# Optimization experiments

Hardware: AMD Instinct MI355X
Metric: run time of the kernel (lower is better)

## Reference

```python
import jax, jax.numpy as jnp
import numpy as np

D = 1024      # model dim
F = 4 * D     # FFN hidden dim
E = 8         # number of experts
TOP_K = 2


def setup_inputs() -> dict:
    key = jax.random.key(0)
    ks = jax.random.split(key, 7)
    s_r = 1.0 / np.sqrt(D)
    s_f = 1.0 / np.sqrt(F)
    return {
        "x": jax.random.normal(ks[0], (2, 2048, D), dtype=jnp.float32),
        "Wr": jax.random.uniform(ks[1], (D, E), jnp.float32, -s_r, s_r),
        "br": jax.random.uniform(ks[2], (E,), jnp.float32, -s_r, s_r),
        "W1": jax.random.uniform(ks[3], (E, D, F), jnp.float32, -s_r, s_r),
        "b1": jax.random.uniform(ks[4], (E, F), jnp.float32, -s_r, s_r),
        "W2": jax.random.uniform(ks[5], (E, F, D), jnp.float32, -s_f, s_f),
        "b2": jax.random.uniform(ks[6], (E, D), jnp.float32, -s_f, s_f),
    }


def reference(x, Wr, br, W1, b1, W2, b2):
    B, S, d = x.shape
    T = B * S
    xf = x.reshape(T, d)                                   # [T, D]
    logits = xf @ Wr + br                                  # [T, E]
    top_vals, top_idx = jax.lax.top_k(logits, TOP_K)       # [T, K]
    rw = jax.nn.softmax(top_vals, axis=-1)                 # softmax over selected experts
    # Dense routing-weight matrix: zero for unselected experts -> same math as masked loop.
    w = jnp.zeros((T, E), dtype=xf.dtype).at[jnp.arange(T)[:, None], top_idx].add(rw)  # [T, E]
    # All-expert FFN (exact GELU to match torch.nn.GELU default).
    h = jax.nn.gelu(jnp.einsum('td,edf->tef', xf, W1) + b1[None], approximate=False)   # [T, E, F]
    y = jnp.einsum('tef,efd->ted', h, W2) + b2[None]       # [T, E, D]
    out = jnp.einsum('te,ted->td', w, y)                   # combine
    return out.reshape(B, S, d)
```

## Files before the change

### kernel.cpp

```cpp
#include <hip/hip_runtime.h>
#include <math.h>


#define T_TOK 4096
#define DMODEL 1024
#define FDIM 4096
#define NEXP 8
#define MAXROWS 9216
#define NRB 72

typedef unsigned short u16;
typedef unsigned int u32;
typedef __attribute__((ext_vector_type(8))) short short8;
typedef __attribute__((ext_vector_type(4))) float f32x4;

constexpr size_t OFF_CTRL   = 0;
constexpr size_t OFF_ROWMAP = 4096;
constexpr size_t OFF_ROWW   = OFF_ROWMAP + (size_t)MAXROWS*4;
constexpr size_t OFF_TKIDX  = OFF_ROWW + (size_t)MAXROWS*4;
constexpr size_t OFF_TKW    = OFF_TKIDX + (size_t)T_TOK*2*4;
constexpr size_t OFF_XB     = 262144;
constexpr size_t OFF_W1T    = OFF_XB + (size_t)T_TOK*DMODEL*2;
constexpr size_t OFF_W2T    = OFF_W1T + (size_t)NEXP*DMODEL*FDIM*2;
constexpr size_t OFF_H      = OFF_W2T + (size_t)NEXP*FDIM*DMODEL*2;
constexpr size_t WS_NEED    = OFF_H + (size_t)MAXROWS*FDIM*2;

__device__ __forceinline__ u16 f2bf(float f) {
  u32 u = __float_as_uint(f);
  u += 0x7FFFu + ((u >> 16) & 1u);
  return (u16)(u >> 16);
}

__device__ __forceinline__ float fast_gelu(float v) {
  float u2 = v * (1.5957691216f + 0.0713548162f * v * v);
  float s = __expf(-u2);
  return v * __builtin_amdgcn_rcpf(1.0f + s);
}

__device__ __forceinline__ void async16(void* lds, const void* g) {
  __builtin_amdgcn_global_load_lds((const __attribute__((address_space(1))) void*)g,
                                   (__attribute__((address_space(3))) void*)lds,
                                   16, 0, 0);
}

__global__ void init_cast_kernel(const float* __restrict__ x, u16* __restrict__ xb,
                                 int* __restrict__ ctrl, int* __restrict__ rowmap) {
  int g = blockIdx.x * 256 + threadIdx.x;
  float4 v = ((const float4*)x)[g];
  u32 p0 = (u32)f2bf(v.x) | ((u32)f2bf(v.y) << 16);
  u32 p1 = (u32)f2bf(v.z) | ((u32)f2bf(v.w) << 16);
  ((uint2*)xb)[g] = make_uint2(p0, p1);
  if (g < NEXP) ctrl[g] = 0;
  if (g < MAXROWS) rowmap[g] = -1;
}

__global__ void router_kernel(const float* __restrict__ x, const float* __restrict__ Wr,
                              const float* __restrict__ br, int* __restrict__ ctrl,
                              int* __restrict__ tk_idx, float* __restrict__ tk_w) {
  int lane = threadIdx.x & 63, w = threadIdx.x >> 6;
  int t = blockIdx.x * 4 + w;
  const float* xt = x + (size_t)t * DMODEL;
  float acc[8] = {0.f,0.f,0.f,0.f,0.f,0.f,0.f,0.f};
  for (int i = 0; i < DMODEL / 64; i++) {
    int d = i * 64 + lane;
    float xv = xt[d];
    float4 w0 = *(const float4*)(Wr + d * 8);
    float4 w1 = *(const float4*)(Wr + d * 8 + 4);
    acc[0] += xv * w0.x; acc[1] += xv * w0.y; acc[2] += xv * w0.z; acc[3] += xv * w0.w;
    acc[4] += xv * w1.x; acc[5] += xv * w1.y; acc[6] += xv * w1.z; acc[7] += xv * w1.w;
  }
  #pragma unroll
  for (int off = 32; off > 0; off >>= 1)
    #pragma unroll
    for (int e = 0; e < 8; e++) acc[e] += __shfl_xor(acc[e], off);
  if (lane == 0) {
    float lg[8];
    #pragma unroll
    for (int e = 0; e < 8; e++) lg[e] = acc[e] + br[e];
    int e0 = 0;
    #pragma unroll
    for (int e = 1; e < 8; e++) if (lg[e] > lg[e0]) e0 = e;
    int e1 = -1;
    #pragma unroll
    for (int e = 0; e < 8; e++) if (e != e0 && (e1 < 0 || lg[e] > lg[e1])) e1 = e;
    float p1 = __expf(lg[e1] - lg[e0]);
    float inv = 1.f / (1.f + p1);
    tk_idx[t*2] = e0; tk_idx[t*2+1] = e1;
    tk_w[t*2] = inv;  tk_w[t*2+1] = p1 * inv;
    atomicAdd(&ctrl[e0], 1); atomicAdd(&ctrl[e1], 1);
  }
}

__global__ void transpose_cast_kernel(const float* __restrict__ in, u16* __restrict__ outp,
                                      int K, int N) {
  __shared__ float tile[64][65];
  int e = blockIdx.z;
  const float* src = in + (size_t)e * K * N;
  u16* dst = outp + (size_t)e * K * N;
  int k0 = blockIdx.y * 64, n0 = blockIdx.x * 64;
  int t = threadIdx.x;
  int kr = t >> 4, nc = (t & 15) * 4;
  #pragma unroll
  for (int rr = 0; rr < 4; rr++) {
    int k = kr + rr * 16;
    float4 v = *(const float4*)(src + (size_t)(k0 + k) * N + n0 + nc);
    tile[nc+0][k] = v.x; tile[nc+1][k] = v.y; tile[nc+2][k] = v.z; tile[nc+3][k] = v.w;
  }
  __syncthreads();
  int n = t >> 2, kc = (t & 3) * 16;
  u32 res[8];
  #pragma unroll
  for (int u = 0; u < 8; u++) {
    u32 lo = f2bf(tile[n][kc + u*2]);
    u32 hi = f2bf(tile[n][kc + u*2 + 1]);
    res[u] = lo | (hi << 16);
  }
  uint4* o = (uint4*)(dst + (size_t)(n0 + n) * K + k0 + kc);
  o[0] = make_uint4(res[0], res[1], res[2], res[3]);
  o[1] = make_uint4(res[4], res[5], res[6], res[7]);
}

__global__ void scan_kernel(int* __restrict__ ctrl) {
  __shared__ int so[9];
  if (threadIdx.x == 0) {
    int o = 0;
    for (int e = 0; e < 8; e++) {
      so[e] = o; ctrl[16 + e] = o;
      o += (ctrl[e] + 127) & ~127;
    }
    so[8] = o; ctrl[24] = o;
    for (int e = 0; e < 8; e++) ctrl[8 + e] = 0;
  }
  __syncthreads();
  int b = threadIdx.x;
  if (b < NRB) {
    int base = b * 128, ex = -1;
    for (int e = 0; e < 8; e++) if (base >= so[e] && base < so[e+1]) ex = e;
    ctrl[32 + b] = ex;
  }
}

__global__ void assign_kernel(const int* __restrict__ tk_idx, const float* __restrict__ tk_w,
                              int* __restrict__ ctrl, int* __restrict__ rowmap,
                              float* __restrict__ roww) {
  int t = blockIdx.x * 256 + threadIdx.x;
  if (t >= T_TOK) return;
  #pragma unroll
  for (int k = 0; k < 2; k++) {
    int e = tk_idx[t*2 + k];
    int slot = atomicAdd(&ctrl[8 + e], 1);
    int r = ctrl[16 + e] + slot;
    rowmap[r] = t;
    roww[r] = tk_w[t*2 + k];
  }
}


__global__ void gemm1_kernel(const u16* __restrict__ xb, const u16* __restrict__ W1t,
                             const float* __restrict__ b1, const int* __restrict__ ctrl,
                             const int* __restrict__ rowmap, u16* __restrict__ h) {
  int rb = blockIdx.y, nb = blockIdx.x;
  int e = ctrl[32 + rb];
  if (e < 0) return;
  __shared__ u16 As[4096];
  __shared__ u16 Bs[4096];
  int tid = threadIdx.x, lane = tid & 63, w = tid >> 6;
  int c0 = w, c1 = w + 4;
  int rA0 = c0*16 + (lane >> 2), rA1 = c1*16 + (lane >> 2);
  int colo = (((lane & 3) ^ ((lane >> 3) & 3))) * 8;
  int t0 = rowmap[rb*128 + rA0]; t0 = t0 < 0 ? 0 : t0;
  int t1 = rowmap[rb*128 + rA1]; t1 = t1 < 0 ? 0 : t1;
  const u16* gA0 = xb + (size_t)t0 * DMODEL + colo;
  const u16* gA1 = xb + (size_t)t1 * DMODEL + colo;
  const u16* We  = W1t + (size_t)e * FDIM * DMODEL;
  const u16* gB0 = We + (size_t)(nb*128 + rA0) * DMODEL + colo;
  const u16* gB1 = We + (size_t)(nb*128 + rA1) * DMODEL + colo;
  u16* lA0 = &As[c0*512]; u16* lA1 = &As[c1*512];
  u16* lB0 = &Bs[c0*512]; u16* lB1 = &Bs[c1*512];
  f32x4 acc[4][4];
  f32x4 z = {0.f, 0.f, 0.f, 0.f};
  #pragma unroll
  for (int i = 0; i < 4; i++)
    #pragma unroll
    for (int j = 0; j < 4; j++) acc[i][j] = z;
  int m0 = (w >> 1) * 64, n0 = (w & 1) * 64, q = lane >> 4, cc = lane & 15;
  int sa = (q ^ ((cc >> 1) & 3)) * 8;
  for (int kb = 0; kb < DMODEL / 32; kb++) {
    async16(lA0, gA0); async16(lA1, gA1);
    async16(lB0, gB0); async16(lB1, gB1);
    gA0 += 32; gA1 += 32; gB0 += 32; gB1 += 32;
    __syncthreads();
    short8 af[4], bf[4];
    #pragma unroll
    for (int i = 0; i < 4; i++) af[i] = *(const short8*)&As[(m0 + i*16 + cc)*32 + sa];
    #pragma unroll
    for (int j = 0; j < 4; j++) bf[j] = *(const short8*)&Bs[(n0 + j*16 + cc)*32 + sa];
    #pragma unroll
    for (int i = 0; i < 4; i++)
      #pragma unroll
      for (int j = 0; j < 4; j++)
        acc[i][j] = __builtin_amdgcn_mfma_f32_16x16x32_bf16(af[i], bf[j], acc[i][j], 0, 0, 0);
    __syncthreads();
  }
  float bias[4];
  #pragma unroll
  for (int j = 0; j < 4; j++) bias[j] = b1[e*FDIM + nb*128 + n0 + j*16 + cc];
  #pragma unroll
  for (int i = 0; i < 4; i++)
    #pragma unroll
    for (int j = 0; j < 4; j++) {
      int col = nb*128 + n0 + j*16 + cc;
      #pragma unroll
      for (int r = 0; r < 4; r++) {
        int row = rb*128 + m0 + i*16 + q*4 + r;
        float v = acc[i][j][r] + bias[j];
        h[(size_t)row * FDIM + col] = f2bf(fast_gelu(v));
      }
    }
}

__global__ void gemm2_kernel(const u16* __restrict__ h, const u16* __restrict__ W2t,
                             const float* __restrict__ b2, const int* __restrict__ ctrl,
                             const int* __restrict__ rowmap, const float* __restrict__ roww,
                             float* __restrict__ out) {
  int rb = blockIdx.y, nb = blockIdx.x, zs = blockIdx.z;
  int e = ctrl[32 + rb];
  if (e < 0) return;
  __shared__ u16 As[4096];
  __shared__ u16 Bs[4096];
  int tid = threadIdx.x, lane = tid & 63, w = tid >> 6;
  int c0 = w, c1 = w + 4;
  int rA0 = c0*16 + (lane >> 2), rA1 = c1*16 + (lane >> 2);
  int colo = (((lane & 3) ^ ((lane >> 3) & 3))) * 8;
  size_t kbase = (size_t)zs * (FDIM / 2);
  const u16* gA0 = h + (size_t)(rb*128 + rA0) * FDIM + kbase + colo;
  const u16* gA1 = h + (size_t)(rb*128 + rA1) * FDIM + kbase + colo;
  const u16* We  = W2t + (size_t)e * DMODEL * FDIM;
  const u16* gB0 = We + (size_t)(nb*128 + rA0) * FDIM + kbase + colo;
  const u16* gB1 = We + (size_t)(nb*128 + rA1) * FDIM + kbase + colo;
  u16* lA0 = &As[c0*512]; u16* lA1 = &As[c1*512];
  u16* lB0 = &Bs[c0*512]; u16* lB1 = &Bs[c1*512];
  f32x4 acc[4][4];
  f32x4 z = {0.f, 0.f, 0.f, 0.f};
  #pragma unroll
  for (int i = 0; i < 4; i++)
    #pragma unroll
    for (int j = 0; j < 4; j++) acc[i][j] = z;
  int m0 = (w >> 1) * 64, n0 = (w & 1) * 64, q = lane >> 4, cc = lane & 15;
  int sa = (q ^ ((cc >> 1) & 3)) * 8;
  for (int kb = 0; kb < FDIM / 2 / 32; kb++) {
    async16(lA0, gA0); async16(lA1, gA1);
    async16(lB0, gB0); async16(lB1, gB1);
    gA0 += 32; gA1 += 32; gB0 += 32; gB1 += 32;
    __syncthreads();
    short8 af[4], bf[4];
    #pragma unroll
    for (int i = 0; i < 4; i++) af[i] = *(const short8*)&As[(m0 + i*16 + cc)*32 + sa];
    #pragma unroll
    for (int j = 0; j < 4; j++) bf[j] = *(const short8*)&Bs[(n0 + j*16 + cc)*32 + sa];
    #pragma unroll
    for (int i = 0; i < 4; i++)
      #pragma unroll
      for (int j = 0; j < 4; j++)
        acc[i][j] = __builtin_amdgcn_mfma_f32_16x16x32_bf16(af[i], bf[j], acc[i][j], 0, 0, 0);
    __syncthreads();
  }
  float bias[4];
  #pragma unroll
  for (int j = 0; j < 4; j++)
    bias[j] = (zs == 0) ? b2[e*DMODEL + nb*128 + n0 + j*16 + cc] : 0.0f;
  #pragma unroll
  for (int i = 0; i < 4; i++)
    #pragma unroll
    for (int r = 0; r < 4; r++) {
      int row = rb*128 + m0 + i*16 + q*4 + r;
      int t = rowmap[row];
      if (t < 0) continue;
      float wgt = roww[row];
      float* orow = out + (size_t)t * DMODEL;
      #pragma unroll
      for (int j = 0; j < 4; j++) {
        int col = nb*128 + n0 + j*16 + cc;
        atomicAdd(orow + col, wgt * (acc[i][j][r] + bias[j]));
      }
    }
}

extern "C" void kernel_launch(void* const* d_in, const int* in_sizes, int n_in,
                              void* d_out, int out_size, void* d_ws, size_t ws_size,
                              hipStream_t stream) {
  const float* x  = (const float*)d_in[0];
  const float* Wr = (const float*)d_in[1];
  const float* br = (const float*)d_in[2];
  const float* W1 = (const float*)d_in[3];
  const float* b1 = (const float*)d_in[4];
  const float* W2 = (const float*)d_in[5];
  const float* b2 = (const float*)d_in[6];
  float* out = (float*)d_out;
  char* ws = (char*)d_ws;
  if (ws_size < WS_NEED) return;

  int*   ctrl   = (int*)(ws + OFF_CTRL);
  int*   rowmap = (int*)(ws + OFF_ROWMAP);
  float* roww   = (float*)(ws + OFF_ROWW);
  int*   tk_idx = (int*)(ws + OFF_TKIDX);
  float* tk_w   = (float*)(ws + OFF_TKW);
  u16*   xb     = (u16*)(ws + OFF_XB);
  u16*   W1t    = (u16*)(ws + OFF_W1T);
  u16*   W2t    = (u16*)(ws + OFF_W2T);
  u16*   hbuf   = (u16*)(ws + OFF_H);

  hipMemsetAsync(out, 0, (size_t)out_size * sizeof(float), stream);
  init_cast_kernel<<<T_TOK*DMODEL/4/256, 256, 0, stream>>>(x, xb, ctrl, rowmap);
  router_kernel<<<T_TOK/4, 256, 0, stream>>>(x, Wr, br, ctrl, tk_idx, tk_w);
  transpose_cast_kernel<<<dim3(FDIM/64, DMODEL/64, NEXP), 256, 0, stream>>>(W1, W1t, DMODEL, FDIM);
  transpose_cast_kernel<<<dim3(DMODEL/64, FDIM/64, NEXP), 256, 0, stream>>>(W2, W2t, FDIM, DMODEL);
  scan_kernel<<<1, 128, 0, stream>>>(ctrl);
  assign_kernel<<<T_TOK/256, 256, 0, stream>>>(tk_idx, tk_w, ctrl, rowmap, roww);
  gemm1_kernel<<<dim3(FDIM/128, NRB), 256, 0, stream>>>(xb, W1t, b1, ctrl, rowmap, hbuf);
  gemm2_kernel<<<dim3(DMODEL/128, NRB, 2), 256, 0, stream>>>(hbuf, W2t, b2, ctrl, rowmap, roww, out);
}
```

Before: 744.3 us.

## Double-buffer GEMM LDS tiles and replace atomic split-K scatter with a combine pass

Both expert GEMMs now use two LDS buffers per operand. Each k-step issues the async global-to-LDS loads for the next tile before running the MFMAs on the current one, and only one barrier remains per iteration. gemm2 drops its two-way split-K and float atomicAdd scatter into the output: it runs the full K loop and writes per-row expert outputs to a y buffer placed over the W1t workspace. A new combine kernel then gathers each token's two rows through a token-to-row map and applies the routing weights, which also removes the output memset. The cost is that gemm2 launches half as many blocks, and there is an extra fp32 write and read of the y buffer.

```diff
diff --git a/kernel.cpp b/kernel.cpp
--- a/kernel.cpp
+++ b/kernel.cpp
@@ -19,11 +19,13 @@
 constexpr size_t OFF_ROWW   = OFF_ROWMAP + (size_t)MAXROWS*4;
 constexpr size_t OFF_TKIDX  = OFF_ROWW + (size_t)MAXROWS*4;
 constexpr size_t OFF_TKW    = OFF_TKIDX + (size_t)T_TOK*2*4;
+constexpr size_t OFF_T2R    = OFF_TKW + (size_t)T_TOK*2*4;
 constexpr size_t OFF_XB     = 262144;
 constexpr size_t OFF_W1T    = OFF_XB + (size_t)T_TOK*DMODEL*2;
 constexpr size_t OFF_W2T    = OFF_W1T + (size_t)NEXP*DMODEL*FDIM*2;
 constexpr size_t OFF_H      = OFF_W2T + (size_t)NEXP*FDIM*DMODEL*2;
 constexpr size_t WS_NEED    = OFF_H + (size_t)MAXROWS*FDIM*2;
+constexpr size_t OFF_Y      = OFF_W1T;
 
 __device__ __forceinline__ u16 f2bf(float f) {
   u32 u = __float_as_uint(f);
@@ -142,7 +144,7 @@
 
 __global__ void assign_kernel(const int* __restrict__ tk_idx, const float* __restrict__ tk_w,
                               int* __restrict__ ctrl, int* __restrict__ rowmap,
-                              float* __restrict__ roww) {
+                              float* __restrict__ roww, int* __restrict__ t2r) {
   int t = blockIdx.x * 256 + threadIdx.x;
   if (t >= T_TOK) return;
   #pragma unroll
@@ -152,6 +154,7 @@
     int r = ctrl[16 + e] + slot;
     rowmap[r] = t;
     roww[r] = tk_w[t*2 + k];
+    t2r[t*2 + k] = r;
   }
 }
 
@@ -162,8 +165,8 @@
   int rb = blockIdx.y, nb = blockIdx.x;
   int e = ctrl[32 + rb];
   if (e < 0) return;
-  __shared__ u16 As[4096];
-  __shared__ u16 Bs[4096];
+  __shared__ u16 As[2][4096];
+  __shared__ u16 Bs[2][4096];
   int tid = threadIdx.x, lane = tid & 63, w = tid >> 6;
   int c0 = w, c1 = w + 4;
   int rA0 = c0*16 + (lane >> 2), rA1 = c1*16 + (lane >> 2);
@@ -175,8 +178,6 @@
   const u16* We  = W1t + (size_t)e * FDIM * DMODEL;
   const u16* gB0 = We + (size_t)(nb*128 + rA0) * DMODEL + colo;
   const u16* gB1 = We + (size_t)(nb*128 + rA1) * DMODEL + colo;
-  u16* lA0 = &As[c0*512]; u16* lA1 = &As[c1*512];
-  u16* lB0 = &Bs[c0*512]; u16* lB1 = &Bs[c1*512];
   f32x4 acc[4][4];
   f32x4 z = {0.f, 0.f, 0.f, 0.f};
   #pragma unroll
@@ -185,22 +186,29 @@
     for (int j = 0; j < 4; j++) acc[i][j] = z;
   int m0 = (w >> 1) * 64, n0 = (w & 1) * 64, q = lane >> 4, cc = lane & 15;
   int sa = (q ^ ((cc >> 1) & 3)) * 8;
-  for (int kb = 0; kb < DMODEL / 32; kb++) {
-    async16(lA0, gA0); async16(lA1, gA1);
-    async16(lB0, gB0); async16(lB1, gB1);
-    gA0 += 32; gA1 += 32; gB0 += 32; gB1 += 32;
+  async16(&As[0][c0*512], gA0); async16(&As[0][c1*512], gA1);
+  async16(&Bs[0][c0*512], gB0); async16(&Bs[0][c1*512], gB1);
+  gA0 += 32; gA1 += 32; gB0 += 32; gB1 += 32;
+  constexpr int NK = DMODEL / 32;
+  for (int kb = 0; kb < NK; kb++) {
+    int cur = kb & 1;
     __syncthreads();
+    if (kb + 1 < NK) {
+      int nxt = cur ^ 1;
+      async16(&As[nxt][c0*512], gA0); async16(&As[nxt][c1*512], gA1);
+      async16(&Bs[nxt][c0*512], gB0); async16(&Bs[nxt][c1*512], gB1);
+      gA0 += 32; gA1 += 32; gB0 += 32; gB1 += 32;
+    }
     short8 af[4], bf[4];
     #pragma unroll
-    for (int i = 0; i < 4; i++) af[i] = *(const short8*)&As[(m0 + i*16 + cc)*32 + sa];
-    #pragma unroll
-    for (int j = 0; j < 4; j++) bf[j] = *(const short8*)&Bs[(n0 + j*16 + cc)*32 + sa];
+    for (int i = 0; i < 4; i++) af[i] = *(const short8*)&As[cur][(m0 + i*16 + cc)*32 + sa];
+    #pragma unroll
+    for (int j = 0; j < 4; j++) bf[j] = *(const short8*)&Bs[cur][(n0 + j*16 + cc)*32 + sa];
     #pragma unroll
     for (int i = 0; i < 4; i++)
       #pragma unroll
       for (int j = 0; j < 4; j++)
         acc[i][j] = __builtin_amdgcn_mfma_f32_16x16x32_bf16(af[i], bf[j], acc[i][j], 0, 0, 0);
-    __syncthreads();
   }
   float bias[4];
   #pragma unroll
@@ -221,25 +229,21 @@
 
 __global__ void gemm2_kernel(const u16* __restrict__ h, const u16* __restrict__ W2t,
                              const float* __restrict__ b2, const int* __restrict__ ctrl,
-                             const int* __restrict__ rowmap, const float* __restrict__ roww,
-                             float* __restrict__ out) {
-  int rb = blockIdx.y, nb = blockIdx.x, zs = blockIdx.z;
+                             float* __restrict__ y) {
+  int rb = blockIdx.y, nb = blockIdx.x;
   int e = ctrl[32 + rb];
   if (e < 0) return;
-  __shared__ u16 As[4096];
-  __shared__ u16 Bs[4096];
+  __shared__ u16 As[2][4096];
+  __shared__ u16 Bs[2][4096];
   int tid = threadIdx.x, lane = tid & 63, w = tid >> 6;
   int c0 = w, c1 = w + 4;
   int rA0 = c0*16 + (lane >> 2), rA1 = c1*16 + (lane >> 2);
   int colo = (((lane & 3) ^ ((lane >> 3) & 3))) * 8;
-  size_t kbase = (size_t)zs * (FDIM / 2);
-  const u16* gA0 = h + (size_t)(rb*128 + rA0) * FDIM + kbase + colo;
-  const u16* gA1 = h + (size_t)(rb*128 + rA1) * FDIM + kbase + colo;
+  const u16* gA0 = h + (size_t)(rb*128 + rA0) * FDIM + colo;
+  const u16* gA1 = h + (size_t)(rb*128 + rA1) * FDIM + colo;
   const u16* We  = W2t + (size_t)e * DMODEL * FDIM;
-  const u16* gB0 = We + (size_t)(nb*128 + rA0) * FDIM + kbase + colo;
-  const u16* gB1 = We + (size_t)(nb*128 + rA1) * FDIM + kbase + colo;
-  u16* lA0 = &As[c0*512]; u16* lA1 = &As[c1*512];
-  u16* lB0 = &Bs[c0*512]; u16* lB1 = &Bs[c1*512];
+  const u16* gB0 = We + (size_t)(nb*128 + rA0) * FDIM + colo;
+  const u16* gB1 = We + (size_t)(nb*128 + rA1) * FDIM + colo;
   f32x4 acc[4][4];
   f32x4 z = {0.f, 0.f, 0.f, 0.f};
   #pragma unroll
@@ -248,42 +252,58 @@
     for (int j = 0; j < 4; j++) acc[i][j] = z;
   int m0 = (w >> 1) * 64, n0 = (w & 1) * 64, q = lane >> 4, cc = lane & 15;
   int sa = (q ^ ((cc >> 1) & 3)) * 8;
-  for (int kb = 0; kb < FDIM / 2 / 32; kb++) {
-    async16(lA0, gA0); async16(lA1, gA1);
-    async16(lB0, gB0); async16(lB1, gB1);
-    gA0 += 32; gA1 += 32; gB0 += 32; gB1 += 32;
+  async16(&As[0][c0*512], gA0); async16(&As[0][c1*512], gA1);
+  async16(&Bs[0][c0*512], gB0); async16(&Bs[0][c1*512], gB1);
+  gA0 += 32; gA1 += 32; gB0 += 32; gB1 += 32;
+  constexpr int NK = FDIM / 32;
+  for (int kb = 0; kb < NK; kb++) {
+    int cur = kb & 1;
     __syncthreads();
+    if (kb + 1 < NK) {
+      int nxt = cur ^ 1;
+      async16(&As[nxt][c0*512], gA0); async16(&As[nxt][c1*512], gA1);
+      async16(&Bs[nxt][c0*512], gB0); async16(&Bs[nxt][c1*512], gB1);
+      gA0 += 32; gA1 += 32; gB0 += 32; gB1 += 32;
+    }
     short8 af[4], bf[4];
     #pragma unroll
-    for (int i = 0; i < 4; i++) af[i] = *(const short8*)&As[(m0 + i*16 + cc)*32 + sa];
-    #pragma unroll
-    for (int j = 0; j < 4; j++) bf[j] = *(const short8*)&Bs[(n0 + j*16 + cc)*32 + sa];
+    for (int i = 0; i < 4; i++) af[i] = *(const short8*)&As[cur][(m0 + i*16 + cc)*32 + sa];
+    #pragma unroll
+    for (int j = 0; j < 4; j++) bf[j] = *(const short8*)&Bs[cur][(n0 + j*16 + cc)*32 + sa];
     #pragma unroll
     for (int i = 0; i < 4; i++)
       #pragma unroll
       for (int j = 0; j < 4; j++)
         acc[i][j] = __builtin_amdgcn_mfma_f32_16x16x32_bf16(af[i], bf[j], acc[i][j], 0, 0, 0);
-    __syncthreads();
   }
   float bias[4];
   #pragma unroll
-  for (int j = 0; j < 4; j++)
-    bias[j] = (zs == 0) ? b2[e*DMODEL + nb*128 + n0 + j*16 + cc] : 0.0f;
+  for (int j = 0; j < 4; j++) bias[j] = b2[e*DMODEL + nb*128 + n0 + j*16 + cc];
   #pragma unroll
   for (int i = 0; i < 4; i++)
     #pragma unroll
     for (int r = 0; r < 4; r++) {
       int row = rb*128 + m0 + i*16 + q*4 + r;
-      int t = rowmap[row];
-      if (t < 0) continue;
-      float wgt = roww[row];
-      float* orow = out + (size_t)t * DMODEL;
+      float* yrow = y + (size_t)row * DMODEL;
       #pragma unroll
       for (int j = 0; j < 4; j++) {
         int col = nb*128 + n0 + j*16 + cc;
-        atomicAdd(orow + col, wgt * (acc[i][j][r] + bias[j]));
+        yrow[col] = acc[i][j][r] + bias[j];
       }
     }
+}
+
+__global__ void combine_kernel(const float* __restrict__ y, const int* __restrict__ t2r,
+                               const float* __restrict__ tk_w, float* __restrict__ out) {
+  int t = blockIdx.x, d4 = threadIdx.x;
+  int r0 = t2r[t*2], r1 = t2r[t*2+1];
+  float w0 = tk_w[t*2], w1 = tk_w[t*2+1];
+  float4 a = ((const float4*)(y + (size_t)r0 * DMODEL))[d4];
+  float4 b = ((const float4*)(y + (size_t)r1 * DMODEL))[d4];
+  float4 o;
+  o.x = w0*a.x + w1*b.x; o.y = w0*a.y + w1*b.y;
+  o.z = w0*a.z + w1*b.z; o.w = w0*a.w + w1*b.w;
+  ((float4*)(out + (size_t)t * DMODEL))[d4] = o;
 }
 
 extern "C" void kernel_launch(void* const* d_in, const int* in_sizes, int n_in,
@@ -305,18 +325,20 @@
   float* roww   = (float*)(ws + OFF_ROWW);
   int*   tk_idx = (int*)(ws + OFF_TKIDX);
   float* tk_w   = (float*)(ws + OFF_TKW);
+  int*   t2r    = (int*)(ws + OFF_T2R);
   u16*   xb     = (u16*)(ws + OFF_XB);
   u16*   W1t    = (u16*)(ws + OFF_W1T);
   u16*   W2t    = (u16*)(ws + OFF_W2T);
   u16*   hbuf   = (u16*)(ws + OFF_H);
-
-  hipMemsetAsync(out, 0, (size_t)out_size * sizeof(float), stream);
+  float* ybuf   = (float*)(ws + OFF_Y);
+
   init_cast_kernel<<<T_TOK*DMODEL/4/256, 256, 0, stream>>>(x, xb, ctrl, rowmap);
   router_kernel<<<T_TOK/4, 256, 0, stream>>>(x, Wr, br, ctrl, tk_idx, tk_w);
   transpose_cast_kernel<<<dim3(FDIM/64, DMODEL/64, NEXP), 256, 0, stream>>>(W1, W1t, DMODEL, FDIM);
   transpose_cast_kernel<<<dim3(DMODEL/64, FDIM/64, NEXP), 256, 0, stream>>>(W2, W2t, FDIM, DMODEL);
   scan_kernel<<<1, 128, 0, stream>>>(ctrl);
-  assign_kernel<<<T_TOK/256, 256, 0, stream>>>(tk_idx, tk_w, ctrl, rowmap, roww);
+  assign_kernel<<<T_TOK/256, 256, 0, stream>>>(tk_idx, tk_w, ctrl, rowmap, roww, t2r);
   gemm1_kernel<<<dim3(FDIM/128, NRB), 256, 0, stream>>>(xb, W1t, b1, ctrl, rowmap, hbuf);
-  gemm2_kernel<<<dim3(DMODEL/128, NRB, 2), 256, 0, stream>>>(hbuf, W2t, b2, ctrl, rowmap, roww, out);
-}
+  gemm2_kernel<<<dim3(DMODEL/128, NRB), 256, 0, stream>>>(hbuf, W2t, b2, ctrl, ybuf);
+  combine_kernel<<<T_TOK, 256, 0, stream>>>(ybuf, t2r, tk_w, out);
+}
```

New measurement: 702.1 us. 5.7% less time.
